# Kernel tuning notes

Measured on AMD Instinct MI355X. Metric: run time of the kernel, lower is better.

The kernel has to match this reference:

```python
import jax, jax.numpy as jnp
import numpy as np

HEADS = 8
HEAD_DIM = 64
GROUPS = 32
EPS = 1e-5


def setup_inputs() -> dict:
    key = jax.random.key(0)
    ks = jax.random.split(key, 8)
    B, C, H, W = 16, 256, 32, 32
    TD = 1024
    inner = HEADS * HEAD_DIM
    return {
        "x": jax.random.normal(ks[0], (B, C, H, W), jnp.float32),
        "embedding": jax.random.normal(ks[1], (B, TD), jnp.float32),
        "norm_w": jnp.ones((C,), jnp.float32),
        "norm_b": jnp.zeros((C,), jnp.float32),
        "in_w": jax.random.normal(ks[2], (3 * inner, C), jnp.float32) * (1.0 / np.sqrt(C)),
        "in_b": jnp.zeros((3 * inner,), jnp.float32),
        "out_w": jax.random.normal(ks[3], (C, inner), jnp.float32) * (1.0 / np.sqrt(inner)),
        "out_b": jnp.zeros((C,), jnp.float32),
        "emb_w": jax.random.normal(ks[4], (C, TD), jnp.float32) * (1.0 / np.sqrt(TD)),
        "emb_b": jnp.zeros((C,), jnp.float32),
    }


def reference(x, embedding, norm_w, norm_b, in_w, in_b, out_w, out_b, emb_w, emb_b):
    b, c, h, w = x.shape
    scale = 1.0 / np.sqrt(HEAD_DIM)
    # GroupNorm over (C//G, H, W) per group
    xg = x.reshape(b, GROUPS, -1)
    mean = xg.mean(-1, keepdims=True)
    var = xg.var(-1, keepdims=True)
    xn = ((xg - mean) * jax.lax.rsqrt(var + EPS)).reshape(b, c, h, w)
    xn = xn * norm_w[:, None, None] + norm_b[:, None, None]
    # 1x1 conv QKV projection: [b, 3*inner, h, w]
    qkv = jnp.einsum('oc,bchw->bohw', in_w, xn) + in_b[:, None, None]
    q, k, v = jnp.split(qkv, 3, axis=1)
    # [b, heads, head_dim, hw]
    q = q.reshape(b, HEADS, HEAD_DIM, h * w)
    k = k.reshape(b, HEADS, HEAD_DIM, h * w)
    v = v.reshape(b, HEADS, HEAD_DIM, h * w)
    attn = jax.nn.softmax(jnp.einsum('bhcm,bhcn->bhmn', q, k) * scale, axis=-1)
    o = jnp.einsum('bhmn,bhcn->bhcm', attn, v)  # [b,h,c,hw]
    o = o.reshape(b, HEADS * HEAD_DIM, h, w)
    out = jnp.einsum('oc,bchw->bohw', out_w, o) + out_b[:, None, None]
    emb = embedding @ emb_w.T + emb_b  # [b, C]
    return out * emb[:, :, None, None] + x
```

## Files before the change

kernel.cpp:

```cpp
#include <hip/hip_runtime.h>

#define DEV __device__ __forceinline__

typedef _Float16 f16;
typedef _Float16 f16x8 __attribute__((ext_vector_type(8)));
typedef _Float16 f16x4 __attribute__((ext_vector_type(4)));
typedef float f32x4 __attribute__((ext_vector_type(4)));
typedef unsigned int u32;

static constexpr int NB = 16;
static constexpr int NC = 256;
static constexpr int HW = 1024;
static constexpr int NG = 32;
static constexpr int CPG = 8;
static constexpr int NH = 8;
static constexpr int HD = 64;
static constexpr int INNER = 512;
static constexpr int TD = 1024;

DEV f32x4 mfma16(f16x8 a, f16x8 b, f32x4 c) {
    return __builtin_amdgcn_mfma_f32_16x16x32_f16(a, b, c, 0, 0, 0);
}

DEV u32 pk2(float a, float b) {
    auto c = __builtin_amdgcn_cvt_pkrtz(a, b);
    return __builtin_bit_cast(u32, c);
}

__global__ void prep_k(const float* __restrict__ x, float* __restrict__ stats,
                       const float* __restrict__ in_w, const float* __restrict__ out_w,
                       f16* __restrict__ w_in, f16* __restrict__ w_out,
                       const float* __restrict__ e, const float* __restrict__ ew,
                       const float* __restrict__ eb, float* __restrict__ embS) {
    int bid = blockIdx.x;
    if (bid < NB * NG) {
        int bg = bid;
        const float4* p = reinterpret_cast<const float4*>(x) + (size_t)bg * (CPG * HW / 4);
        float s = 0.f, ss = 0.f;
        for (int i = threadIdx.x; i < CPG * HW / 4; i += 256) {
            float4 v = p[i];
            s  += v.x + v.y + v.z + v.w;
            ss += v.x * v.x + v.y * v.y + v.z * v.z + v.w * v.w;
        }
        #pragma unroll
        for (int o = 32; o > 0; o >>= 1) {
            s  += __shfl_xor(s, o);
            ss += __shfl_xor(ss, o);
        }
        __shared__ float rs[4], rss[4];
        int wid = threadIdx.x >> 6;
        if ((threadIdx.x & 63) == 0) { rs[wid] = s; rss[wid] = ss; }
        __syncthreads();
        if (threadIdx.x == 0) {
            s  = rs[0] + rs[1] + rs[2] + rs[3];
            ss = rss[0] + rss[1] + rss[2] + rss[3];
            const float inv_n = 1.f / (float)(CPG * HW);
            float mean = s * inv_n;
            float var  = ss * inv_n - mean * mean;
            stats[bg * 2]     = mean;
            stats[bg * 2 + 1] = rsqrtf(var + 1e-5f);
        }
    } else if (bid < NB * NG + 512) {
        int i = (bid - NB * NG) * 256 + threadIdx.x;
        const int N1 = 3 * INNER * NC / 4;
        float4 v;
        f16* dst;
        if (i < N1) { v = reinterpret_cast<const float4*>(in_w)[i];       dst = w_in + (size_t)i * 4; }
        else        { v = reinterpret_cast<const float4*>(out_w)[i - N1]; dst = w_out + (size_t)(i - N1) * 4; }
        f16x4 h4 = {(f16)v.x, (f16)v.y, (f16)v.z, (f16)v.w};
        *reinterpret_cast<f16x4*>(dst) = h4;
    } else {
        int u = bid - (NB * NG + 512);
        int b = u >> 6;
        int co = ((u & 63) << 2) + (threadIdx.x >> 6);
        int lane = threadIdx.x & 63;
        const float4* ep = reinterpret_cast<const float4*>(e + (size_t)b * TD);
        const float4* wp = reinterpret_cast<const float4*>(ew + (size_t)co * TD);
        float s = 0.f;
        for (int t = lane; t < TD / 4; t += 64) {
            float4 a = ep[t], w = wp[t];
            s += a.x * w.x + a.y * w.y + a.z * w.z + a.w * w.w;
        }
        #pragma unroll
        for (int o = 32; o > 0; o >>= 1) s += __shfl_xor(s, o);
        if (lane == 0) embS[b * NC + co] = s + eb[co];
    }
}

__global__ void gn_apply_k(const float* __restrict__ x, const float* __restrict__ stats,
                           const float* __restrict__ nw, const float* __restrict__ nb,
                           f16* __restrict__ xnT) {
    int b = blockIdx.y;
    int m = blockIdx.x * 64 + (threadIdx.x & 63);
    int c0 = (threadIdx.x >> 6) * 64;
    const float* xb = x + (size_t)b * NC * HW + m;
    f16* op = xnT + ((size_t)b * HW + m) * NC + c0;
    #pragma unroll
    for (int cc = 0; cc < 64; cc += 8) {
        int cg = c0 + cc;
        float mean = stats[(b * NG + (cg >> 3)) * 2];
        float rstd = stats[(b * NG + (cg >> 3)) * 2 + 1];
        f16x8 h;
        #pragma unroll
        for (int j = 0; j < 8; ++j) {
            int c = cg + j;
            float v = xb[(size_t)c * HW];
            h[j] = (f16)(((v - mean) * rstd) * nw[c] + nb[c]);
        }
        *reinterpret_cast<f16x8*>(op + cc) = h;
    }
}

__global__ __launch_bounds__(256) void gemm_qkv_k(
        const f16* __restrict__ wA, const f16* __restrict__ xnT,
        const float* __restrict__ bias,
        f16* __restrict__ qT, f16* __restrict__ kT, f16* __restrict__ vv) {
    int bid = blockIdx.x;
    int u = (bid & 7) * 192 + (bid >> 3);
    int o0 = (u % 12) * 128;
    int rr = u / 12;
    int m0 = (rr & 7) * 128;
    int b  = rr >> 3;
    int wid  = threadIdx.x >> 6;
    int lane = threadIdx.x & 63;
    int wr = (wid >> 1) * 64, wc = (wid & 1) * 64;
    int lr = lane & 15, lg = lane >> 4;

    const f16* A  = wA  + (size_t)(o0 + wr + lr) * NC + lg * 8;
    const f16* Bp = xnT + ((size_t)b * HW + m0 + wc + lr) * NC + lg * 8;

    const f32x4 fzero = {0.f, 0.f, 0.f, 0.f};
    f32x4 acc[4][4];
    #pragma unroll
    for (int i = 0; i < 4; ++i) {
        #pragma unroll
        for (int j = 0; j < 4; ++j) acc[i][j] = fzero;
    }

    for (int k0 = 0; k0 < NC; k0 += 32) {
        f16x8 af[4], bf[4];
        #pragma unroll
        for (int i = 0; i < 4; ++i)
            af[i] = *reinterpret_cast<const f16x8*>(A + (size_t)i * 16 * NC + k0);
        #pragma unroll
        for (int j = 0; j < 4; ++j)
            bf[j] = *reinterpret_cast<const f16x8*>(Bp + (size_t)j * 16 * NC + k0);
        #pragma unroll
        for (int i = 0; i < 4; ++i) {
            #pragma unroll
            for (int j = 0; j < 4; ++j)
                acc[i][j] = mfma16(af[i], bf[j], acc[i][j]);
        }
    }

    const float SL = 0.18033688011112042f;
    #pragma unroll
    for (int i = 0; i < 4; ++i) {
        int ob = o0 + wr + i * 16 + lg * 4;
        #pragma unroll
        for (int j = 0; j < 4; ++j) {
            int m = m0 + wc + j * 16 + lr;
            float v0 = acc[i][j][0] + bias[ob];
            float v1 = acc[i][j][1] + bias[ob + 1];
            float v2 = acc[i][j][2] + bias[ob + 2];
            float v3 = acc[i][j][3] + bias[ob + 3];
            if (ob < INNER) {
                int h = ob >> 6, c = ob & 63;
                f16x4 pk = {(f16)v0, (f16)v1, (f16)v2, (f16)v3};
                *reinterpret_cast<f16x4*>(qT + (((size_t)(b * NH + h) * HW + m) * HD + c)) = pk;
            } else if (ob < 2 * INNER) {
                int oo = ob - INNER;
                int h = oo >> 6, c = oo & 63;
                f16x4 pk = {(f16)(v0 * SL), (f16)(v1 * SL), (f16)(v2 * SL), (f16)(v3 * SL)};
                *reinterpret_cast<f16x4*>(kT + (((size_t)(b * NH + h) * HW + m) * HD + c)) = pk;
            } else {
                int oo = ob - 2 * INNER;
                int h = oo >> 6, c = oo & 63;
                f16* vp = vv + ((size_t)(b * NH + h) * HD + c) * HW + m;
                vp[0]      = (f16)v0;
                vp[HW]     = (f16)v1;
                vp[2 * HW] = (f16)v2;
                vp[3 * HW] = (f16)v3;
            }
        }
    }
}

DEV void load_kv(const f16* __restrict__ kp0, const f16* __restrict__ vp,
                 int n0, int lr, int lg, f16x8 (&kf)[2][2], f16x8 (&vf)[4]) {
    const f16* p0 = kp0 + (size_t)n0 * HD;
    kf[0][0] = *reinterpret_cast<const f16x8*>(p0);
    kf[0][1] = *reinterpret_cast<const f16x8*>(p0 + 32);
    kf[1][0] = *reinterpret_cast<const f16x8*>(p0 + 4 * HD);
    kf[1][1] = *reinterpret_cast<const f16x8*>(p0 + 4 * HD + 32);
    #pragma unroll
    for (int dt = 0; dt < 4; ++dt)
        vf[dt] = *reinterpret_cast<const f16x8*>(
            vp + (size_t)(dt * 16 + lr) * HW + n0 + lg * 8);
}

DEV void attn_tile(const f16x8 (&kf)[2][2], const f16x8 (&vf)[4],
                   const f16x8 (&qf)[4][2],
                   f32x4 (&oa)[4][4], float (&mr)[4], float (&lsl)[4]) {
    const float THR = 11.0f;
    const f32x4 fzero = {0.f, 0.f, 0.f, 0.f};
    #pragma unroll
    for (int qt = 0; qt < 4; ++qt) {
        f32x4 sc0 = fzero, sc1 = fzero;
        __builtin_amdgcn_s_setprio(1);
        sc0 = mfma16(kf[0][0], qf[qt][0], sc0);
        sc0 = mfma16(kf[0][1], qf[qt][1], sc0);
        sc1 = mfma16(kf[1][0], qf[qt][0], sc1);
        sc1 = mfma16(kf[1][1], qf[qt][1], sc1);
        __builtin_amdgcn_s_setprio(0);

        float m0 = fmaxf(fmaxf(sc0[0], sc0[1]), fmaxf(sc0[2], sc0[3]));
        float m1 = fmaxf(fmaxf(sc1[0], sc1[1]), fmaxf(sc1[2], sc1[3]));
        float pmax = fmaxf(m0, m1);
        if (__any(pmax - mr[qt] > THR)) {
            float pm = pmax;
            pm = fmaxf(pm, __shfl_xor(pm, 16));
            pm = fmaxf(pm, __shfl_xor(pm, 32));
            float mn = fmaxf(mr[qt], pm);
            float f = exp2f(mr[qt] - mn);
            mr[qt] = mn;
            lsl[qt] *= f;
            #pragma unroll
            for (int dt = 0; dt < 4; ++dt)
                #pragma unroll
                for (int r = 0; r < 4; ++r) oa[qt][dt][r] *= f;
        }
        float p[8];
        #pragma unroll
        for (int r = 0; r < 4; ++r) p[r]     = exp2f(sc0[r] - mr[qt]);
        #pragma unroll
        for (int r = 0; r < 4; ++r) p[4 + r] = exp2f(sc1[r] - mr[qt]);
        lsl[qt] += ((p[0] + p[1]) + (p[2] + p[3])) + ((p[4] + p[5]) + (p[6] + p[7]));

        union { u32 u[4]; f16x8 v; } pfu;
        pfu.u[0] = pk2(p[0], p[1]);
        pfu.u[1] = pk2(p[2], p[3]);
        pfu.u[2] = pk2(p[4], p[5]);
        pfu.u[3] = pk2(p[6], p[7]);

        __builtin_amdgcn_s_setprio(1);
        #pragma unroll
        for (int dt = 0; dt < 4; ++dt)
            oa[qt][dt] = mfma16(vf[dt], pfu.v, oa[qt][dt]);
        __builtin_amdgcn_s_setprio(0);
    }
}

__global__ __launch_bounds__(256) void attn_k(
        const f16* __restrict__ qT, const f16* __restrict__ kT, const f16* __restrict__ vv,
        f16* __restrict__ oT) {
    int u = ((blockIdx.x & 7) << 6) | (blockIdx.x >> 3);
    int bh = u >> 2;
    int mt = u & 3;
    int b = bh >> 3, h = bh & 7;
    int wid = threadIdx.x >> 6;
    int lane = threadIdx.x & 63;
    int lr = lane & 15, lg = lane >> 4;
    int mw = mt * 256 + wid * 64;

    const f16* qp = qT + (size_t)bh * HW * HD;
    const f16* kp0 = kT + (size_t)bh * HW * HD
                   + (size_t)(8 * (lr >> 2) + (lr & 3)) * HD + lg * 8;
    const f16* vp = vv + (size_t)bh * HD * HW;

    f16x8 qf[4][2];
    #pragma unroll
    for (int qt = 0; qt < 4; ++qt)
        #pragma unroll
        for (int ks2 = 0; ks2 < 2; ++ks2)
            qf[qt][ks2] = *reinterpret_cast<const f16x8*>(
                qp + (size_t)(mw + qt * 16 + lr) * HD + ks2 * 32 + lg * 8);

    const f32x4 fzero = {0.f, 0.f, 0.f, 0.f};
    f32x4 oa[4][4];
    #pragma unroll
    for (int qt = 0; qt < 4; ++qt)
        #pragma unroll
        for (int dt = 0; dt < 4; ++dt) oa[qt][dt] = fzero;
    float mr[4]  = {-1e30f, -1e30f, -1e30f, -1e30f};
    float lsl[4] = {0.f, 0.f, 0.f, 0.f};

    f16x8 kfA[2][2], vfA[4], kfB[2][2], vfB[4];
    load_kv(kp0, vp, 0, lr, lg, kfA, vfA);
    for (int n0 = 0; n0 < HW; n0 += 64) {
        load_kv(kp0, vp, n0 + 32, lr, lg, kfB, vfB);
        attn_tile(kfA, vfA, qf, oa, mr, lsl);
        if (n0 + 64 < HW) load_kv(kp0, vp, n0 + 64, lr, lg, kfA, vfA);
        attn_tile(kfB, vfB, qf, oa, mr, lsl);
    }

    #pragma unroll
    for (int qt = 0; qt < 4; ++qt) {
        float t = lsl[qt];
        t += __shfl_xor(t, 16);
        t += __shfl_xor(t, 32);
        float inv = 1.f / t;
        int m = mw + qt * 16 + lr;
        f16* op = oT + ((size_t)b * HW + m) * INNER + h * HD;
        #pragma unroll
        for (int dt = 0; dt < 4; ++dt) {
            f16x4 o4;
            #pragma unroll
            for (int r = 0; r < 4; ++r) o4[r] = (f16)(oa[qt][dt][r] * inv);
            *reinterpret_cast<f16x4*>(op + dt * 16 + lg * 4) = o4;
        }
    }
}

__global__ __launch_bounds__(256) void gemm_out_k(
        const f16* __restrict__ wA, const f16* __restrict__ oT,
        const float* __restrict__ bias, const float* __restrict__ embS,
        const float* __restrict__ x, float* __restrict__ out) {
    int bid = blockIdx.x;
    int u = (bid & 7) * 64 + (bid >> 3);
    int o0 = (u & 3) * 64;
    int rr = u >> 2;
    int m0 = (rr & 7) * 128;
    int b  = rr >> 3;
    int wid  = threadIdx.x >> 6;
    int lane = threadIdx.x & 63;
    int wr = (wid >> 1) * 32, wc = (wid & 1) * 64;
    int lr = lane & 15, lg = lane >> 4;

    const f16* A  = wA + (size_t)(o0 + wr + lr) * INNER + lg * 8;
    const f16* Bp = oT + ((size_t)b * HW + m0 + wc + lr) * INNER + lg * 8;

    const f32x4 fzero = {0.f, 0.f, 0.f, 0.f};
    f32x4 acc[2][4];
    #pragma unroll
    for (int i = 0; i < 2; ++i) {
        #pragma unroll
        for (int j = 0; j < 4; ++j) acc[i][j] = fzero;
    }

    for (int k0 = 0; k0 < INNER; k0 += 32) {
        f16x8 af[2], bf[4];
        #pragma unroll
        for (int i = 0; i < 2; ++i)
            af[i] = *reinterpret_cast<const f16x8*>(A + (size_t)i * 16 * INNER + k0);
        #pragma unroll
        for (int j = 0; j < 4; ++j)
            bf[j] = *reinterpret_cast<const f16x8*>(Bp + (size_t)j * 16 * INNER + k0);
        #pragma unroll
        for (int i = 0; i < 2; ++i) {
            #pragma unroll
            for (int j = 0; j < 4; ++j)
                acc[i][j] = mfma16(af[i], bf[j], acc[i][j]);
        }
    }

    #pragma unroll
    for (int i = 0; i < 2; ++i) {
        int ob = o0 + wr + i * 16 + lg * 4;
        #pragma unroll
        for (int j = 0; j < 4; ++j) {
            int m = m0 + wc + j * 16 + lr;
            #pragma unroll
            for (int r = 0; r < 4; ++r) {
                int o = ob + r;
                size_t idx = ((size_t)b * NC + o) * HW + m;
                out[idx] = (acc[i][j][r] + bias[o]) * embS[b * NC + o] + x[idx];
            }
        }
    }
}

extern "C" void kernel_launch(void* const* d_in, const int* in_sizes, int n_in,
                              void* d_out, int out_size, void* d_ws, size_t ws_size,
                              hipStream_t stream) {
    const float* x     = (const float*)d_in[0];
    const float* emb   = (const float*)d_in[1];
    const float* nw    = (const float*)d_in[2];
    const float* nbi   = (const float*)d_in[3];
    const float* in_w  = (const float*)d_in[4];
    const float* in_b  = (const float*)d_in[5];
    const float* out_w = (const float*)d_in[6];
    const float* out_b = (const float*)d_in[7];
    const float* emb_w = (const float*)d_in[8];
    const float* emb_b = (const float*)d_in[9];

    char* p = (char*)d_ws;
    f16* xnT   = (f16*)p;   p += (size_t)NB * HW * NC * 2;
    f16* w_in  = (f16*)p;   p += (size_t)3 * INNER * NC * 2;
    f16* w_out = (f16*)p;   p += (size_t)NC * INNER * 2;
    float* stats = (float*)p; p += (size_t)NB * NG * 2 * 4;
    float* embS  = (float*)p; p += (size_t)NB * NC * 4;
    f16* qT = (f16*)p;      p += (size_t)NB * NH * HW * HD * 2;
    f16* kT = (f16*)p;      p += (size_t)NB * NH * HW * HD * 2;
    f16* vv = (f16*)p;      p += (size_t)NB * NH * HW * HD * 2;
    f16* oT = (f16*)p;

    prep_k<<<NB * NG + 512 + 1024, 256, 0, stream>>>(x, stats, in_w, out_w, w_in, w_out,
                                                     emb, emb_w, emb_b, embS);
    gn_apply_k<<<dim3(HW / 64, NB), 256, 0, stream>>>(x, stats, nw, nbi, xnT);
    gemm_qkv_k<<<1536, 256, 0, stream>>>(w_in, xnT, in_b, qT, kT, vv);
    attn_k<<<512, 256, 0, stream>>>(qT, kT, vv, oT);
    gemm_out_k<<<512, 256, 0, stream>>>(w_out, oT, out_b, embS, x, (float*)d_out);
}
```

Before: 169.0 us.

## Software-pipeline GEMM and attention loads with sched barriers and native exp2

Restructures the QKV and output GEMM k-loops into explicit double-buffered register prefetch, with sched_barrier fences that keep the compiler from merging loads and MFMAs. The attention K/V loop is deepened to a four-stage register prefetch. The softmax exp2f calls are replaced by the hardware exp2 builtin, and launch bounds request 2 blocks per CU. The aim is to hide global-load latency behind MFMA work and cut exp cost. In exchange it raises register pressure and could cause spills or lower occupancy.

```diff
diff --git a/kernel.cpp b/kernel.cpp
--- a/kernel.cpp
+++ b/kernel.cpp
@@ -1,6 +1,7 @@
 #include <hip/hip_runtime.h>
 
 #define DEV __device__ __forceinline__
+#define SB __builtin_amdgcn_sched_barrier(0)
 
 typedef _Float16 f16;
 typedef _Float16 f16x8 __attribute__((ext_vector_type(8)));
@@ -26,6 +27,7 @@
     auto c = __builtin_amdgcn_cvt_pkrtz(a, b);
     return __builtin_bit_cast(u32, c);
 }
+DEV float fexp2(float x) { return __builtin_amdgcn_exp2f(x); }
 
 __global__ void prep_k(const float* __restrict__ x, float* __restrict__ stats,
                        const float* __restrict__ in_w, const float* __restrict__ out_w,
@@ -111,7 +113,24 @@
     }
 }
 
-__global__ __launch_bounds__(256) void gemm_qkv_k(
+DEV void ld_ab4(const f16* __restrict__ A, const f16* __restrict__ Bp, int k0, int stride,
+                f16x8 (&af)[4], f16x8 (&bf)[4]) {
+    #pragma unroll
+    for (int i = 0; i < 4; ++i)
+        af[i] = *reinterpret_cast<const f16x8*>(A + (size_t)i * 16 * stride + k0);
+    #pragma unroll
+    for (int j = 0; j < 4; ++j)
+        bf[j] = *reinterpret_cast<const f16x8*>(Bp + (size_t)j * 16 * stride + k0);
+}
+DEV void mm44(const f16x8 (&af)[4], const f16x8 (&bf)[4], f32x4 (&acc)[4][4]) {
+    #pragma unroll
+    for (int i = 0; i < 4; ++i)
+        #pragma unroll
+        for (int j = 0; j < 4; ++j)
+            acc[i][j] = mfma16(af[i], bf[j], acc[i][j]);
+}
+
+__global__ __launch_bounds__(256, 2) void gemm_qkv_k(
         const f16* __restrict__ wA, const f16* __restrict__ xnT,
         const float* __restrict__ bias,
         f16* __restrict__ qT, f16* __restrict__ kT, f16* __restrict__ vv) {
@@ -132,25 +151,19 @@
     const f32x4 fzero = {0.f, 0.f, 0.f, 0.f};
     f32x4 acc[4][4];
     #pragma unroll
-    for (int i = 0; i < 4; ++i) {
+    for (int i = 0; i < 4; ++i)
         #pragma unroll
         for (int j = 0; j < 4; ++j) acc[i][j] = fzero;
-    }
-
-    for (int k0 = 0; k0 < NC; k0 += 32) {
-        f16x8 af[4], bf[4];
-        #pragma unroll
-        for (int i = 0; i < 4; ++i)
-            af[i] = *reinterpret_cast<const f16x8*>(A + (size_t)i * 16 * NC + k0);
-        #pragma unroll
-        for (int j = 0; j < 4; ++j)
-            bf[j] = *reinterpret_cast<const f16x8*>(Bp + (size_t)j * 16 * NC + k0);
-        #pragma unroll
-        for (int i = 0; i < 4; ++i) {
-            #pragma unroll
-            for (int j = 0; j < 4; ++j)
-                acc[i][j] = mfma16(af[i], bf[j], acc[i][j]);
-        }
+
+    f16x8 afA[4], bfA[4], afB[4], bfB[4];
+    ld_ab4(A, Bp, 0, NC, afA, bfA); SB;
+    #pragma unroll 1
+    for (int g = 0; g < 4; ++g) {
+        int k0 = g * 64;
+        ld_ab4(A, Bp, k0 + 32, NC, afB, bfB); SB;
+        mm44(afA, bfA, acc); SB;
+        if (g < 3) { ld_ab4(A, Bp, k0 + 64, NC, afA, bfA); } SB;
+        mm44(afB, bfB, acc); SB;
     }
 
     const float SL = 0.18033688011112042f;
@@ -222,7 +235,7 @@
             pm = fmaxf(pm, __shfl_xor(pm, 16));
             pm = fmaxf(pm, __shfl_xor(pm, 32));
             float mn = fmaxf(mr[qt], pm);
-            float f = exp2f(mr[qt] - mn);
+            float f = fexp2(mr[qt] - mn);
             mr[qt] = mn;
             lsl[qt] *= f;
             #pragma unroll
@@ -232,9 +245,9 @@
         }
         float p[8];
         #pragma unroll
-        for (int r = 0; r < 4; ++r) p[r]     = exp2f(sc0[r] - mr[qt]);
-        #pragma unroll
-        for (int r = 0; r < 4; ++r) p[4 + r] = exp2f(sc1[r] - mr[qt]);
+        for (int r = 0; r < 4; ++r) p[r]     = fexp2(sc0[r] - mr[qt]);
+        #pragma unroll
+        for (int r = 0; r < 4; ++r) p[4 + r] = fexp2(sc1[r] - mr[qt]);
         lsl[qt] += ((p[0] + p[1]) + (p[2] + p[3])) + ((p[4] + p[5]) + (p[6] + p[7]));
 
         union { u32 u[4]; f16x8 v; } pfu;
@@ -251,7 +264,7 @@
     }
 }
 
-__global__ __launch_bounds__(256) void attn_k(
+__global__ __launch_bounds__(256, 2) void attn_k(
         const f16* __restrict__ qT, const f16* __restrict__ kT, const f16* __restrict__ vv,
         f16* __restrict__ oT) {
     int u = ((blockIdx.x & 7) << 6) | (blockIdx.x >> 3);
@@ -285,14 +298,27 @@
     float mr[4]  = {-1e30f, -1e30f, -1e30f, -1e30f};
     float lsl[4] = {0.f, 0.f, 0.f, 0.f};
 
-    f16x8 kfA[2][2], vfA[4], kfB[2][2], vfB[4];
-    load_kv(kp0, vp, 0, lr, lg, kfA, vfA);
-    for (int n0 = 0; n0 < HW; n0 += 64) {
-        load_kv(kp0, vp, n0 + 32, lr, lg, kfB, vfB);
-        attn_tile(kfA, vfA, qf, oa, mr, lsl);
-        if (n0 + 64 < HW) load_kv(kp0, vp, n0 + 64, lr, lg, kfA, vfA);
-        attn_tile(kfB, vfB, qf, oa, mr, lsl);
-    }
+    f16x8 kfA[2][2], vfA[4], kfB[2][2], vfB[4], kfC[2][2], vfC[4], kfD[2][2], vfD[4];
+    load_kv(kp0, vp, 0,  lr, lg, kfA, vfA); SB;
+    load_kv(kp0, vp, 32, lr, lg, kfB, vfB); SB;
+    load_kv(kp0, vp, 64, lr, lg, kfC, vfC); SB;
+    #pragma unroll 1
+    for (int g = 0; g < 7; ++g) {
+        int n0 = g * 128;
+        load_kv(kp0, vp, n0 + 96,  lr, lg, kfD, vfD); SB;
+        attn_tile(kfA, vfA, qf, oa, mr, lsl); SB;
+        load_kv(kp0, vp, n0 + 128, lr, lg, kfA, vfA); SB;
+        attn_tile(kfB, vfB, qf, oa, mr, lsl); SB;
+        load_kv(kp0, vp, n0 + 160, lr, lg, kfB, vfB); SB;
+        attn_tile(kfC, vfC, qf, oa, mr, lsl); SB;
+        load_kv(kp0, vp, n0 + 192, lr, lg, kfC, vfC); SB;
+        attn_tile(kfD, vfD, qf, oa, mr, lsl); SB;
+    }
+    load_kv(kp0, vp, 992, lr, lg, kfD, vfD); SB;
+    attn_tile(kfA, vfA, qf, oa, mr, lsl); SB;
+    attn_tile(kfB, vfB, qf, oa, mr, lsl); SB;
+    attn_tile(kfC, vfC, qf, oa, mr, lsl); SB;
+    attn_tile(kfD, vfD, qf, oa, mr, lsl);
 
     #pragma unroll
     for (int qt = 0; qt < 4; ++qt) {
@@ -333,25 +359,34 @@
     const f32x4 fzero = {0.f, 0.f, 0.f, 0.f};
     f32x4 acc[2][4];
     #pragma unroll
-    for (int i = 0; i < 2; ++i) {
+    for (int i = 0; i < 2; ++i)
         #pragma unroll
         for (int j = 0; j < 4; ++j) acc[i][j] = fzero;
-    }
-
-    for (int k0 = 0; k0 < INNER; k0 += 32) {
-        f16x8 af[2], bf[4];
+
+    f16x8 afA[2], bfA[4], afB[2], bfB[4];
+    auto ld = [&](int k0, f16x8 (&af)[2], f16x8 (&bf)[4]) {
         #pragma unroll
         for (int i = 0; i < 2; ++i)
             af[i] = *reinterpret_cast<const f16x8*>(A + (size_t)i * 16 * INNER + k0);
         #pragma unroll
         for (int j = 0; j < 4; ++j)
             bf[j] = *reinterpret_cast<const f16x8*>(Bp + (size_t)j * 16 * INNER + k0);
-        #pragma unroll
-        for (int i = 0; i < 2; ++i) {
+    };
+    auto mm = [&](const f16x8 (&af)[2], const f16x8 (&bf)[4]) {
+        #pragma unroll
+        for (int i = 0; i < 2; ++i)
             #pragma unroll
             for (int j = 0; j < 4; ++j)
                 acc[i][j] = mfma16(af[i], bf[j], acc[i][j]);
-        }
+    };
+    ld(0, afA, bfA); SB;
+    #pragma unroll 1
+    for (int g = 0; g < 8; ++g) {
+        int k0 = g * 64;
+        ld(k0 + 32, afB, bfB); SB;
+        mm(afA, bfA); SB;
+        if (g < 7) { ld(k0 + 64, afA, bfA); } SB;
+        mm(afB, bfB); SB;
     }
 
     #pragma unroll
```

Measured after the change: 171.5 us. About the same (+1.5%).
